# Performance work log

Measured on AMD Instinct MI355X. Metric: run time of the kernel, lower is better.

## Reference

```python
import jax, jax.numpy as jnp
import numpy as np

IN_CAPS, OUT_CAPS, OUT_DIM = 32, 10, 16


def squash(s):
    # s: [B, out_caps, out_dim]
    sq = jnp.sum(s * s, axis=2)              # [B, out_caps]
    mod = jnp.sqrt(sq)
    scale = sq / (1.0 + sq) / mod            # matches torch: sqrmod/(1+sqrmod)/mod
    return scale[..., None] * s


def setup_inputs() -> dict:
    key = jax.random.key(0)
    k1, k2 = jax.random.split(key)
    B, in_dim = 4096, 288
    caps_output = jax.random.normal(k1, (B, IN_CAPS, in_dim), dtype=jnp.float32)
    # W initialized uniform(-1/32, 1/32) in the original; scale randn similarly small
    W = jax.random.uniform(k2, (IN_CAPS, in_dim, OUT_CAPS * OUT_DIM),
                           dtype=jnp.float32, minval=-1.0 / 32, maxval=1.0 / 32)
    b = jnp.zeros((IN_CAPS, OUT_CAPS), dtype=jnp.float32)
    return {"caps_output": caps_output, "W": W, "b": b}


def reference(caps_output, W, b):
    B = caps_output.shape[0]
    # caps_output.unsqueeze(2).matmul(W): per-input-capsule matmul
    u = jnp.einsum('bni,nio->bno', caps_output, W)          # [B, 32, 160]
    u = u.reshape(B, IN_CAPS, OUT_CAPS, OUT_DIM)            # [B, 32, 10, 16]

    c = jax.nn.softmax(b, axis=1)                           # [32, 10]
    s = jnp.einsum('no,bnod->bod', c, u)                    # [B, 10, 16]
    v = squash(s)

    b_batch = jnp.broadcast_to(b, (B, IN_CAPS, OUT_CAPS))
    for _ in range(3):
        # agreement: <u_predict, v>
        b_batch = b_batch + jnp.einsum('bnod,bod->bno', u, v)
        c = jax.nn.softmax(b_batch, axis=-1)                # [B, 32, 10]
        s = jnp.einsum('bno,bnod->bod', c, u)
        v = squash(s)
    return v
```

## Files before the change

kernel.cpp:

```cpp
#include <hip/hip_runtime.h>
#include <hip/hip_bf16.h>

#define IN_CAPS 32
#define OUT_CAPS 10
#define OUT_DIM 16
#define NOUT 160
#define KDIM 288
#define BATCH 4096
#define KSTEPS 9
#define CTILES 10
#define USTR 169

typedef __bf16 bf16x8 __attribute__((ext_vector_type(8)));
typedef float  f32x4  __attribute__((ext_vector_type(4)));

__global__ __launch_bounds__(256) void prep_w(const float* __restrict__ W,
                                              __bf16* __restrict__ Wf) {
    int f = blockIdx.x * 256 + threadIdx.x;
    int j    = f & 7;
    int l    = (f >> 3) & 63;
    int rest = f >> 9;
    int c    = rest % CTILES;
    int tnk  = rest / CTILES;
    int ks   = tnk % KSTEPS;
    int n    = tnk / KSTEPS;
    int k    = ks * 32 + (l >> 4) * 8 + j;
    int col  = c * 16 + (l & 15);
    Wf[f] = (__bf16)W[(n * KDIM + k) * NOUT + col];
}

__global__ __launch_bounds__(256, 2) void gemm_u(const float* __restrict__ caps,
                                                 const __bf16* __restrict__ Wf,
                                                 __bf16* __restrict__ u) {
    const int n       = blockIdx.y;
    const int wave    = threadIdx.x >> 6;
    const int lane    = threadIdx.x & 63;
    const int rowbase = (blockIdx.x * 4 + wave) * 64;
    const int lm      = lane & 15;
    const int lk      = lane >> 4;

    f32x4 acc[4][CTILES];
#pragma unroll
    for (int mt = 0; mt < 4; ++mt)
#pragma unroll
        for (int ct = 0; ct < CTILES; ++ct)
            acc[mt][ct] = (f32x4){0.f, 0.f, 0.f, 0.f};

    const __bf16* wfn = Wf + (size_t)n * (KSTEPS * CTILES * 512);

    for (int ks = 0; ks < KSTEPS; ++ks) {
        bf16x8 afr[4];
#pragma unroll
        for (int mt = 0; mt < 4; ++mt) {
            const float* src = caps + (size_t)(rowbase + mt * 16 + lm) * (IN_CAPS * KDIM)
                                    + n * KDIM + ks * 32 + lk * 8;
            f32x4 x0 = *(const f32x4*)(src);
            f32x4 x1 = *(const f32x4*)(src + 4);
            bf16x8 a;
            a[0] = (__bf16)x0[0]; a[1] = (__bf16)x0[1];
            a[2] = (__bf16)x0[2]; a[3] = (__bf16)x0[3];
            a[4] = (__bf16)x1[0]; a[5] = (__bf16)x1[1];
            a[6] = (__bf16)x1[2]; a[7] = (__bf16)x1[3];
            afr[mt] = a;
        }
        const __bf16* wks = wfn + (size_t)ks * (CTILES * 512) + lane * 8;
#pragma unroll
        for (int ct = 0; ct < CTILES; ++ct) {
            bf16x8 bfr = *(const bf16x8*)(wks + ct * 512);
#pragma unroll
            for (int mt = 0; mt < 4; ++mt)
                acc[mt][ct] = __builtin_amdgcn_mfma_f32_16x16x32_bf16(afr[mt], bfr, acc[mt][ct], 0, 0, 0);
        }
    }

#pragma unroll
    for (int mt = 0; mt < 4; ++mt)
#pragma unroll
        for (int ct = 0; ct < CTILES; ++ct)
#pragma unroll
            for (int r = 0; r < 4; ++r) {
                int row = rowbase + mt * 16 + lk * 4 + r;
                int col = ct * 16 + lm;
                u[((size_t)row * IN_CAPS + n) * NOUT + col] = (__bf16)acc[mt][ct][r];
            }
}

__global__ __launch_bounds__(256) void routing(const __bf16* __restrict__ u,
                                               const float* __restrict__ bbias,
                                               float* __restrict__ out) {
    __shared__ float ul[IN_CAPS * USTR];
    __shared__ float bl[IN_CAPS * OUT_CAPS];
    __shared__ float cs[IN_CAPS * OUT_CAPS];
    __shared__ float ss[NOUT];
    __shared__ float vs[NOUT];
    __shared__ float scale_s[OUT_CAPS];

    const int b = blockIdx.x;
    const int t = threadIdx.x;
    const __bf16* ub = u + (size_t)b * (IN_CAPS * NOUT);

    for (int cc = t; cc < 640; cc += 256) {
        int n = cc / 20;
        int rem = cc - n * 20;
        uint4 raw = *(const uint4*)(ub + cc * 8);
        bf16x8 bv = __builtin_bit_cast(bf16x8, raw);
#pragma unroll
        for (int j = 0; j < 8; ++j) ul[n * USTR + rem * 8 + j] = (float)bv[j];
    }
    for (int p = t; p < IN_CAPS * OUT_CAPS; p += 256) bl[p] = bbias[p];
    __syncthreads();

    for (int it = 0; it < 4; ++it) {
        if (it > 0) {
            for (int p = t; p < IN_CAPS * OUT_CAPS; p += 256) {
                int n = p & 31;
                int o = p >> 5;
                float a = 0.f;
#pragma unroll
                for (int d = 0; d < 16; ++d)
                    a += ul[n * USTR + o * 16 + d] * vs[o * 16 + d];
                bl[n * 10 + o] += a;
            }
            __syncthreads();
        }
        if (t < IN_CAPS) {
            float m = bl[t * 10];
#pragma unroll
            for (int o = 1; o < 10; ++o) m = fmaxf(m, bl[t * 10 + o]);
            float e[10];
            float sum = 0.f;
#pragma unroll
            for (int o = 0; o < 10; ++o) { e[o] = __expf(bl[t * 10 + o] - m); sum += e[o]; }
            float inv = 1.0f / sum;
#pragma unroll
            for (int o = 0; o < 10; ++o) cs[t * 10 + o] = e[o] * inv;
        }
        __syncthreads();
        if (t < NOUT) {
            int o = t >> 4;
            float acc = 0.f;
#pragma unroll
            for (int n = 0; n < IN_CAPS; ++n)
                acc += cs[n * 10 + o] * ul[n * USTR + t];
            ss[t] = acc;
        }
        __syncthreads();
        if (t < OUT_CAPS) {
            float sq = 0.f;
#pragma unroll
            for (int d = 0; d < 16; ++d) { float x = ss[t * 16 + d]; sq += x * x; }
            scale_s[t] = sq / ((1.0f + sq) * sqrtf(sq));
        }
        __syncthreads();
        if (t < NOUT) vs[t] = scale_s[t >> 4] * ss[t];
        __syncthreads();
    }

    if (t < NOUT) out[(size_t)b * NOUT + t] = vs[t];
}

extern "C" void kernel_launch(void* const* d_in, const int* in_sizes, int n_in,
                              void* d_out, int out_size, void* d_ws, size_t ws_size,
                              hipStream_t stream) {
    const float* caps  = (const float*)d_in[0];
    const float* W     = (const float*)d_in[1];
    const float* bbias = (const float*)d_in[2];
    float* out = (float*)d_out;

    __bf16* Wf = (__bf16*)d_ws;
    __bf16* u  = (__bf16*)((char*)d_ws + 2949120);

    prep_w<<<dim3(5760), dim3(256), 0, stream>>>(W, Wf);
    gemm_u<<<dim3(16, 32), dim3(256), 0, stream>>>(caps, Wf, u);
    routing<<<dim3(BATCH), dim3(256), 0, stream>>>(u, bbias, out);
}
```

Before: 78.36 us.

## Halve GEMM row tile per wave and pack two batch items per routing block

The GEMM kernel now gives each wave 32 rows instead of 64, doubles the grid to 1024 blocks, and asks for 4 blocks per SM so more waves are in flight. The routing kernel handles two batch elements per 256-thread block, each on its own 128-thread group with separate shared arrays, so fewer threads sit idle. In exchange, each W fragment feeds fewer MFMAs and is reloaded more often. Routing shared memory roughly doubles per block, which may cap how many blocks fit at once.

New measurement: 86.73 us. 10.7% more time.

```diff
diff --git a/kernel.cpp b/kernel.cpp
--- a/kernel.cpp
+++ b/kernel.cpp
@@ -29,19 +29,19 @@
     Wf[f] = (__bf16)W[(n * KDIM + k) * NOUT + col];
 }
 
-__global__ __launch_bounds__(256, 2) void gemm_u(const float* __restrict__ caps,
+__global__ __launch_bounds__(256, 4) void gemm_u(const float* __restrict__ caps,
                                                  const __bf16* __restrict__ Wf,
                                                  __bf16* __restrict__ u) {
     const int n       = blockIdx.y;
     const int wave    = threadIdx.x >> 6;
     const int lane    = threadIdx.x & 63;
-    const int rowbase = (blockIdx.x * 4 + wave) * 64;
+    const int rowbase = blockIdx.x * 128 + wave * 32;
     const int lm      = lane & 15;
     const int lk      = lane >> 4;
 
-    f32x4 acc[4][CTILES];
+    f32x4 acc[2][CTILES];
 #pragma unroll
-    for (int mt = 0; mt < 4; ++mt)
+    for (int mt = 0; mt < 2; ++mt)
 #pragma unroll
         for (int ct = 0; ct < CTILES; ++ct)
             acc[mt][ct] = (f32x4){0.f, 0.f, 0.f, 0.f};
@@ -49,9 +49,9 @@
     const __bf16* wfn = Wf + (size_t)n * (KSTEPS * CTILES * 512);
 
     for (int ks = 0; ks < KSTEPS; ++ks) {
-        bf16x8 afr[4];
+        bf16x8 afr[2];
 #pragma unroll
-        for (int mt = 0; mt < 4; ++mt) {
+        for (int mt = 0; mt < 2; ++mt) {
             const float* src = caps + (size_t)(rowbase + mt * 16 + lm) * (IN_CAPS * KDIM)
                                     + n * KDIM + ks * 32 + lk * 8;
             f32x4 x0 = *(const f32x4*)(src);
@@ -68,13 +68,13 @@
         for (int ct = 0; ct < CTILES; ++ct) {
             bf16x8 bfr = *(const bf16x8*)(wks + ct * 512);
 #pragma unroll
-            for (int mt = 0; mt < 4; ++mt)
+            for (int mt = 0; mt < 2; ++mt)
                 acc[mt][ct] = __builtin_amdgcn_mfma_f32_16x16x32_bf16(afr[mt], bfr, acc[mt][ct], 0, 0, 0);
         }
     }
 
 #pragma unroll
-    for (int mt = 0; mt < 4; ++mt)
+    for (int mt = 0; mt < 2; ++mt)
 #pragma unroll
         for (int ct = 0; ct < CTILES; ++ct)
 #pragma unroll
@@ -88,75 +88,77 @@
 __global__ __launch_bounds__(256) void routing(const __bf16* __restrict__ u,
                                                const float* __restrict__ bbias,
                                                float* __restrict__ out) {
-    __shared__ float ul[IN_CAPS * USTR];
-    __shared__ float bl[IN_CAPS * OUT_CAPS];
-    __shared__ float cs[IN_CAPS * OUT_CAPS];
-    __shared__ float ss[NOUT];
-    __shared__ float vs[NOUT];
-    __shared__ float scale_s[OUT_CAPS];
+    __shared__ float ul[2][IN_CAPS * USTR];
+    __shared__ float bl[2][IN_CAPS * OUT_CAPS];
+    __shared__ float cs[2][IN_CAPS * OUT_CAPS];
+    __shared__ float ss[2][NOUT];
+    __shared__ float vs[2][NOUT];
+    __shared__ float scale_s[2][OUT_CAPS];
 
-    const int b = blockIdx.x;
-    const int t = threadIdx.x;
-    const __bf16* ub = u + (size_t)b * (IN_CAPS * NOUT);
+    const int t  = threadIdx.x;
+    const int gb = t >> 7;
+    const int g  = t & 127;
+    const size_t b = (size_t)blockIdx.x * 2 + gb;
+    const __bf16* ub = u + b * (IN_CAPS * NOUT);
 
-    for (int cc = t; cc < 640; cc += 256) {
+    for (int cc = g; cc < 640; cc += 128) {
         int n = cc / 20;
         int rem = cc - n * 20;
         uint4 raw = *(const uint4*)(ub + cc * 8);
         bf16x8 bv = __builtin_bit_cast(bf16x8, raw);
 #pragma unroll
-        for (int j = 0; j < 8; ++j) ul[n * USTR + rem * 8 + j] = (float)bv[j];
+        for (int j = 0; j < 8; ++j) ul[gb][n * USTR + rem * 8 + j] = (float)bv[j];
     }
-    for (int p = t; p < IN_CAPS * OUT_CAPS; p += 256) bl[p] = bbias[p];
+    for (int p = g; p < IN_CAPS * OUT_CAPS; p += 128) bl[gb][p] = bbias[p];
     __syncthreads();
 
     for (int it = 0; it < 4; ++it) {
         if (it > 0) {
-            for (int p = t; p < IN_CAPS * OUT_CAPS; p += 256) {
+            for (int p = g; p < IN_CAPS * OUT_CAPS; p += 128) {
                 int n = p & 31;
                 int o = p >> 5;
                 float a = 0.f;
 #pragma unroll
                 for (int d = 0; d < 16; ++d)
-                    a += ul[n * USTR + o * 16 + d] * vs[o * 16 + d];
-                bl[n * 10 + o] += a;
+                    a += ul[gb][n * USTR + o * 16 + d] * vs[gb][o * 16 + d];
+                bl[gb][n * 10 + o] += a;
             }
             __syncthreads();
         }
-        if (t < IN_CAPS) {
-            float m = bl[t * 10];
+        if (g < IN_CAPS) {
+            float m = bl[gb][g * 10];
 #pragma unroll
-            for (int o = 1; o < 10; ++o) m = fmaxf(m, bl[t * 10 + o]);
+            for (int o = 1; o < 10; ++o) m = fmaxf(m, bl[gb][g * 10 + o]);
             float e[10];
             float sum = 0.f;
 #pragma unroll
-            for (int o = 0; o < 10; ++o) { e[o] = __expf(bl[t * 10 + o] - m); sum += e[o]; }
+            for (int o = 0; o < 10; ++o) { e[o] = __expf(bl[gb][g * 10 + o] - m); sum += e[o]; }
             float inv = 1.0f / sum;
 #pragma unroll
-            for (int o = 0; o < 10; ++o) cs[t * 10 + o] = e[o] * inv;
+            for (int o = 0; o < 10; ++o) cs[gb][g * 10 + o] = e[o] * inv;
         }
         __syncthreads();
-        if (t < NOUT) {
-            int o = t >> 4;
+        for (int p = g; p < NOUT; p += 128) {
+            int o = p >> 4;
             float acc = 0.f;
 #pragma unroll
             for (int n = 0; n < IN_CAPS; ++n)
-                acc += cs[n * 10 + o] * ul[n * USTR + t];
-            ss[t] = acc;
+                acc += cs[gb][n * 10 + o] * ul[gb][n * USTR + p];
+            ss[gb][p] = acc;
         }
         __syncthreads();
-        if (t < OUT_CAPS) {
+        if (g < OUT_CAPS) {
             float sq = 0.f;
 #pragma unroll
-            for (int d = 0; d < 16; ++d) { float x = ss[t * 16 + d]; sq += x * x; }
-            scale_s[t] = sq / ((1.0f + sq) * sqrtf(sq));
+            for (int d = 0; d < 16; ++d) { float x = ss[gb][g * 16 + d]; sq += x * x; }
+            scale_s[gb][g] = sq / ((1.0f + sq) * sqrtf(sq));
         }
         __syncthreads();
-        if (t < NOUT) vs[t] = scale_s[t >> 4] * ss[t];
+        for (int p = g; p < NOUT; p += 128) vs[gb][p] = scale_s[gb][p >> 4] * ss[gb][p];
         __syncthreads();
     }
 
-    if (t < NOUT) out[(size_t)b * NOUT + t] = vs[t];
+    for (int p = g; p < NOUT; p += 128) out[b * NOUT + p] = vs[gb][p];
 }
 
 extern "C" void kernel_launch(void* const* d_in, const int* in_sizes, int n_in,
@@ -171,6 +173,6 @@
     __bf16* u  = (__bf16*)((char*)d_ws + 2949120);
 
     prep_w<<<dim3(5760), dim3(256), 0, stream>>>(W, Wf);
-    gemm_u<<<dim3(16, 32), dim3(256), 0, stream>>>(caps, Wf, u);
-    routing<<<dim3(BATCH), dim3(256), 0, stream>>>(u, bbias, out);
+    gemm_u<<<dim3(32, 32), dim3(256), 0, stream>>>(caps, Wf, u);
+    routing<<<dim3(BATCH / 2), dim3(256), 0, stream>>>(u, bbias, out);
 }
```
